# Kernel tuning notes

Hardware: AMD Instinct MI355X
Metric: run time of the kernel (lower is better)

## Reference

```python
import jax, jax.numpy as jnp
import numpy as np

N_BINS = 18
TEMP = 0.01  # n_phases > 1e7 so effective_temperature = 0.01 (same as init default)
EPS = 1e-10  # fp16=False
PI = np.pi


def setup_inputs() -> dict:
    key = jax.random.key(0)
    k1, k2 = jax.random.split(key)
    B, C, P, A, S, T = 4, 8, 20, 30, 4, 2048
    phase = jax.random.uniform(k1, (B, C, P, S, T), jnp.float32, -PI, PI)
    amplitude = jax.random.uniform(k2, (B, C, A, S, T), jnp.float32, 0.0, 1.0)
    return {"phase": phase, "amplitude": amplitude}


def reference(phase, amplitude):
    # phase:     (B, C, Fp, S, T)
    # amplitude: (B, C, Fa, S, T)
    edges = jnp.linspace(-PI, PI, N_BINS + 1).astype(phase.dtype)
    centers = (edges[1:] + edges[:-1]) * 0.5  # (N,)

    # Soft phase binning: circular distance to each bin center, softmax over bins.
    diff = phase[..., None] - centers  # (B, C, Fp, S, T, N)
    diff = jnp.fmod(diff + PI, 2.0 * PI) - PI  # torch.fmod = truncated mod = jnp.fmod
    weights = jax.nn.softmax(-jnp.abs(diff) / TEMP, axis=-1)  # (B, C, Fp, S, T, N)

    # Amplitude-weighted histogram: contract over time.
    # dist: (B, C, Fp, Fa, S, N)
    dist = jnp.einsum('bcpstn,bcast->bcpasn', weights, amplitude)

    # Normalize to a distribution over bins, clamp, Shannon entropy.
    p = dist / (dist.sum(axis=-1, keepdims=True) + EPS)
    p = jnp.maximum(p, EPS)
    neg_entropy = (p * jnp.log(p)).sum(axis=-1)  # (B, C, Fp, Fa, S)

    mi = 1.0 + neg_entropy / jnp.log(jnp.asarray(N_BINS, dtype=p.dtype))
    # -> (B, C, S, Fp, Fa) to match torch output layout
    return jnp.transpose(mi, (0, 1, 4, 2, 3))
```

## Files before the change

kernel.cpp:

```cpp
#include <hip/hip_runtime.h>
#include <math.h>
#include <stdint.h>

#define BB 4
#define CC 8
#define PP 20
#define AA 30
#define SS 4
#define TT 2048
#define NB 18

#define TC 128
#define NCH (TT / TC)
#define PG 2
#define NPG (PP / PG)
#define WSTR 132
#define WROWS 19
#define NTH 128

#define BAR() do { asm volatile("s_waitcnt lgkmcnt(0)" ::: "memory"); \
                   __builtin_amdgcn_s_barrier(); } while (0)

typedef _Float16 half4_t __attribute__((ext_vector_type(4)));
typedef _Float16 half8_t __attribute__((ext_vector_type(8)));
typedef float f32x16 __attribute__((ext_vector_type(16)));

__device__ __forceinline__ void weight_top2(float x, int& n0, int& n1,
                                            float& w0, float& w1)
{
    const float PI_F  = 3.14159265358979323846f;
    const float INV_H = 2.8647913f;
    float u = (x + PI_F) * INV_H;
    n0 = (int)floorf(u);
    n0 = n0 < 0 ? 0 : (n0 > NB - 1 ? NB - 1 : n0);
    float f  = u - (float)n0 - 0.5f;
    float af = fabsf(f);
    n1 = n0 + (f >= 0.0f ? 1 : -1);
    float e;
    if (n1 < 0) {
        e = 0.0f; n1 = NB;
    } else {
        if (n1 == NB) n1 = 0;
        e = __expf(fmaf(af, 69.81317008f, -34.90658504f));
    }
    w0 = __builtin_amdgcn_rcpf(1.0f + e);
    w1 = 1.0f - w0;
}

__global__ __launch_bounds__(NTH)
void mi_fused_kernel(const float* __restrict__ phase,
                     const float* __restrict__ amp,
                     float* __restrict__ out)
{
    __shared__ _Float16 Wl[PG][WROWS * WSTR];
    __shared__ _Float16 ampT[2][AA * WSTR];

    const int tid = threadIdx.x;
    const int bid = blockIdx.x;
    const int x   = bid & 7;
    const int kk  = bid >> 3;
    const int pg  = kk % NPG;
    const int g   = x + 8 * (kk / NPG);
    const int s   = g & (SS - 1);
    const int bc  = g >> 2;

    const int wv   = tid >> 6;
    const int lane = tid & 63;
    const int mrow = lane & 31;
    const int mlh  = lane >> 5;
    const int arow = mrow < WROWS ? mrow : (WROWS - 1);
    const int brow = mrow < AA    ? mrow : (AA - 1);

    const int p = pg * PG + wv;
    const float* am  = amp   + (size_t)bc * (AA * SS * TT) + (size_t)s * TT;
    const float* phw = phase + ((size_t)(bc * PP + p) * SS + s) * TT;
    float*       op  = out   + ((size_t)(bc * SS + s) * PP + p) * AA;

    {
        uint2* wz = (uint2*)&Wl[wv][0];
        for (int i = lane; i < 627; i += 64) wz[i] = make_uint2(0u, 0u);
    }
    #pragma unroll
    for (int j = 0; j < 8; ++j) {
        int q = tid + j * NTH;
        int a = q >> 5, tq = q & 31;
        if (a < AA) {
            const float4 v = *(const float4*)&am[(size_t)a * (SS * TT) + tq * 4];
            half4_t h = { (_Float16)v.x, (_Float16)v.y, (_Float16)v.z, (_Float16)v.w };
            *(half4_t*)&ampT[0][a * WSTR + tq * 4] = h;
        }
    }
    float2 ph2 = *(const float2*)&phw[lane * 2];
    BAR();

    f32x16 acc0 = {}, acc1 = {};
    int pn0[2], pn1[2];

    for (int c = 0; c < NCH; ++c) {
        const int cb = c & 1, tb = cb ^ 1;

        float2 nph2 = {};
        float4 stg[8];
        if (c + 1 < NCH) {
            nph2 = *(const float2*)&phw[(c + 1) * TC + lane * 2];
            #pragma unroll
            for (int j = 0; j < 8; ++j) {
                int q = tid + j * NTH;
                int a = q >> 5, tq = q & 31;
                int ac = a < AA ? a : (AA - 1);
                stg[j] = *(const float4*)&am[(size_t)ac * (SS * TT) + (c + 1) * TC + tq * 4];
            }
        }

        #pragma unroll
        for (int j = 0; j < 2; ++j) {
            int col = lane * 2 + j;
            if (c > 0) {
                Wl[wv][pn0[j] * WSTR + col] = (_Float16)0.0f;
                Wl[wv][pn1[j] * WSTR + col] = (_Float16)0.0f;
            }
            int n0, n1; float w0, w1;
            weight_top2(j == 0 ? ph2.x : ph2.y, n0, n1, w0, w1);
            Wl[wv][n0 * WSTR + col] = (_Float16)w0;
            Wl[wv][n1 * WSTR + col] = (_Float16)w1;
            pn0[j] = n0; pn1[j] = n1;
        }

        __builtin_amdgcn_s_setprio(1);
        #pragma unroll
        for (int ks = 0; ks < 8; ++ks) {
            int t0 = ks * 16 + mlh * 8;
            const _Float16* Ab = &Wl[wv][arow * WSTR + t0];
            const _Float16* Bb = &ampT[cb][brow * WSTR + t0];
            half4_t a0 = *(const half4_t*)Ab;
            half4_t a1 = *(const half4_t*)(Ab + 4);
            half4_t b0 = *(const half4_t*)Bb;
            half4_t b1 = *(const half4_t*)(Bb + 4);
            half8_t av = __builtin_shufflevector(a0, a1, 0, 1, 2, 3, 4, 5, 6, 7);
            half8_t bv = __builtin_shufflevector(b0, b1, 0, 1, 2, 3, 4, 5, 6, 7);
            if (ks & 1) acc1 = __builtin_amdgcn_mfma_f32_32x32x16_f16(av, bv, acc1, 0, 0, 0);
            else        acc0 = __builtin_amdgcn_mfma_f32_32x32x16_f16(av, bv, acc0, 0, 0, 0);
        }
        __builtin_amdgcn_s_setprio(0);

        if (c + 1 < NCH) {
            #pragma unroll
            for (int j = 0; j < 8; ++j) {
                int q = tid + j * NTH;
                int a = q >> 5, tq = q & 31;
                if (a < AA) {
                    half4_t h = { (_Float16)stg[j].x, (_Float16)stg[j].y,
                                  (_Float16)stg[j].z, (_Float16)stg[j].w };
                    *(half4_t*)&ampT[tb][a * WSTR + tq * 4] = h;
                }
            }
        }
        ph2 = nph2;
        BAR();
    }

    f32x16 acc = acc0 + acc1;
    float* dmp = (float*)&Wl[wv][0];
    #pragma unroll
    for (int r = 0; r < 16; ++r) {
        int row = (r & 3) + 8 * (r >> 2) + 4 * mlh;
        if (row < NB) dmp[row * 33 + mrow] = acc[r];
    }
    if (lane < AA) {
        float v[NB], tot = 0.0f;
        #pragma unroll
        for (int n = 0; n < NB; ++n) { v[n] = dmp[n * 33 + lane]; tot += v[n]; }
        float inv = 1.0f / (tot + 1e-10f);
        float ne = 0.0f;
        #pragma unroll
        for (int n = 0; n < NB; ++n) {
            float pv = fmaxf(v[n] * inv, 1e-10f);
            ne += pv * logf(pv);
        }
        op[lane] = 1.0f + ne * 0.345975362f;
    }
}

extern "C" void kernel_launch(void* const* d_in, const int* in_sizes, int n_in,
                              void* d_out, int out_size, void* d_ws, size_t ws_size,
                              hipStream_t stream)
{
    const float* phase = (const float*)d_in[0];
    const float* amp   = (const float*)d_in[1];
    float* out = (float*)d_out;
    hipLaunchKernelGGL(mi_fused_kernel, dim3(BB * CC * SS * NPG), dim3(NTH),
                       0, stream, phase, amp, out);
}
```

Before: 30.59 us.

## Split time chunk across two waves per phase row with LDS reduction

```diff
diff --git a/kernel.cpp b/kernel.cpp
--- a/kernel.cpp
+++ b/kernel.cpp
@@ -16,7 +16,7 @@
 #define NPG (PP / PG)
 #define WSTR 132
 #define WROWS 19
-#define NTH 128
+#define NTH 256
 
 #define BAR() do { asm volatile("s_waitcnt lgkmcnt(0)" ::: "memory"); \
                    __builtin_amdgcn_s_barrier(); } while (0)
@@ -47,13 +47,13 @@
     w1 = 1.0f - w0;
 }
 
-__global__ __launch_bounds__(NTH)
+__global__ __launch_bounds__(NTH, 5)
 void mi_fused_kernel(const float* __restrict__ phase,
                      const float* __restrict__ amp,
                      float* __restrict__ out)
 {
-    __shared__ _Float16 Wl[PG][WROWS * WSTR];
-    __shared__ _Float16 ampT[2][AA * WSTR];
+    __shared__ __align__(16) _Float16 Wl[PG][WROWS * WSTR];
+    __shared__ __align__(16) _Float16 ampT[2][AA * WSTR];
 
     const int tid = threadIdx.x;
     const int bid = blockIdx.x;
@@ -64,24 +64,25 @@
     const int s   = g & (SS - 1);
     const int bc  = g >> 2;
 
-    const int wv   = tid >> 6;
+    const int w    = tid >> 6;
+    const int wv   = w & 1;
+    const int kh   = w >> 1;
     const int lane = tid & 63;
     const int mrow = lane & 31;
     const int mlh  = lane >> 5;
     const int arow = mrow < WROWS ? mrow : (WROWS - 1);
     const int brow = mrow < AA    ? mrow : (AA - 1);
+    const int col  = kh * 64 + lane;
 
     const int p = pg * PG + wv;
     const float* am  = amp   + (size_t)bc * (AA * SS * TT) + (size_t)s * TT;
     const float* phw = phase + ((size_t)(bc * PP + p) * SS + s) * TT;
     float*       op  = out   + ((size_t)(bc * SS + s) * PP + p) * AA;
 
-    {
-        uint2* wz = (uint2*)&Wl[wv][0];
-        for (int i = lane; i < 627; i += 64) wz[i] = make_uint2(0u, 0u);
-    }
+    for (int i = tid; i < 2 * 627; i += NTH)
+        ((uint2*)Wl)[i] = make_uint2(0u, 0u);
     #pragma unroll
-    for (int j = 0; j < 8; ++j) {
+    for (int j = 0; j < 4; ++j) {
         int q = tid + j * NTH;
         int a = q >> 5, tq = q & 31;
         if (a < AA) {
@@ -90,21 +91,21 @@
             *(half4_t*)&ampT[0][a * WSTR + tq * 4] = h;
         }
     }
-    float2 ph2 = *(const float2*)&phw[lane * 2];
+    float phv = phw[col];
     BAR();
 
     f32x16 acc0 = {}, acc1 = {};
-    int pn0[2], pn1[2];
+    int pn0 = 0, pn1 = 0;
 
     for (int c = 0; c < NCH; ++c) {
         const int cb = c & 1, tb = cb ^ 1;
 
-        float2 nph2 = {};
-        float4 stg[8];
+        float nphv = 0.0f;
+        float4 stg[4];
         if (c + 1 < NCH) {
-            nph2 = *(const float2*)&phw[(c + 1) * TC + lane * 2];
+            nphv = phw[(c + 1) * TC + col];
             #pragma unroll
-            for (int j = 0; j < 8; ++j) {
+            for (int j = 0; j < 4; ++j) {
                 int q = tid + j * NTH;
                 int a = q >> 5, tq = q & 31;
                 int ac = a < AA ? a : (AA - 1);
@@ -112,24 +113,22 @@
             }
         }
 
-        #pragma unroll
-        for (int j = 0; j < 2; ++j) {
-            int col = lane * 2 + j;
-            if (c > 0) {
-                Wl[wv][pn0[j] * WSTR + col] = (_Float16)0.0f;
-                Wl[wv][pn1[j] * WSTR + col] = (_Float16)0.0f;
-            }
+        if (c > 0) {
+            Wl[wv][pn0 * WSTR + col] = (_Float16)0.0f;
+            Wl[wv][pn1 * WSTR + col] = (_Float16)0.0f;
+        }
+        {
             int n0, n1; float w0, w1;
-            weight_top2(j == 0 ? ph2.x : ph2.y, n0, n1, w0, w1);
+            weight_top2(phv, n0, n1, w0, w1);
             Wl[wv][n0 * WSTR + col] = (_Float16)w0;
             Wl[wv][n1 * WSTR + col] = (_Float16)w1;
-            pn0[j] = n0; pn1[j] = n1;
+            pn0 = n0; pn1 = n1;
         }
 
         __builtin_amdgcn_s_setprio(1);
         #pragma unroll
-        for (int ks = 0; ks < 8; ++ks) {
-            int t0 = ks * 16 + mlh * 8;
+        for (int ks = 0; ks < 4; ++ks) {
+            int t0 = kh * 64 + ks * 16 + mlh * 8;
             const _Float16* Ab = &Wl[wv][arow * WSTR + t0];
             const _Float16* Bb = &ampT[cb][brow * WSTR + t0];
             half4_t a0 = *(const half4_t*)Ab;
@@ -145,7 +144,7 @@
 
         if (c + 1 < NCH) {
             #pragma unroll
-            for (int j = 0; j < 8; ++j) {
+            for (int j = 0; j < 4; ++j) {
                 int q = tid + j * NTH;
                 int a = q >> 5, tq = q & 31;
                 if (a < AA) {
@@ -155,21 +154,28 @@
                 }
             }
         }
-        ph2 = nph2;
+        phv = nphv;
         BAR();
     }
 
     f32x16 acc = acc0 + acc1;
-    float* dmp = (float*)&Wl[wv][0];
+    float* dmp = (float*)((char*)&Wl[wv][0] + kh * 2376);
     #pragma unroll
     for (int r = 0; r < 16; ++r) {
         int row = (r & 3) + 8 * (r >> 2) + 4 * mlh;
         if (row < NB) dmp[row * 33 + mrow] = acc[r];
     }
-    if (lane < AA) {
+    BAR();
+
+    if (kh == 0 && lane < AA) {
+        const float* d0 = (const float*)&Wl[wv][0];
+        const float* d1 = (const float*)((char*)&Wl[wv][0] + 2376);
         float v[NB], tot = 0.0f;
         #pragma unroll
-        for (int n = 0; n < NB; ++n) { v[n] = dmp[n * 33 + lane]; tot += v[n]; }
+        for (int n = 0; n < NB; ++n) {
+            v[n] = d0[n * 33 + lane] + d1[n * 33 + lane];
+            tot += v[n];
+        }
         float inv = 1.0f / (tot + 1e-10f);
         float ne = 0.0f;
         #pragma unroll
```

New measurement: 29.00 us. 5.2% less time.
